# Kernel tuning notes

Measured on AMD Instinct MI355X. Metric: run time of the kernel, lower is better.

## Reference

```python
import jax, jax.numpy as jnp
import numpy as np

# LIFRefracParameters defaults (norse)
TAU_SYN_INV = 200.0   # 1/5e-3
TAU_MEM_INV = 100.0   # 1/1e-2
V_LEAK = 0.0
V_TH = 1.0
V_RESET = 0.0
ALPHA = 100.0
RHO_RESET = 5.0
DT = 0.001


@jax.custom_vjp
def heaviside(x):
    # forward: hard threshold; backward: super-spike surrogate
    return (x > 0).astype(x.dtype)

def _heaviside_fwd(x):
    return heaviside(x), x

def _heaviside_bwd(x, g):
    return (g / (ALPHA * jnp.abs(x) + 1.0) ** 2,)

heaviside.defvjp(_heaviside_fwd, _heaviside_bwd)


def setup_inputs() -> dict:
    key = jax.random.key(0)
    ks = jax.random.split(key, 8)
    B, H, I = 32768, 256, 128
    return {
        "input_tensor": jax.random.normal(ks[0], (B, I), dtype=jnp.float32),
        "z": jax.random.uniform(ks[1], (B, H), dtype=jnp.float32),
        "v": jax.random.normal(ks[2], (B, H), dtype=jnp.float32),
        "i": jax.random.normal(ks[3], (B, H), dtype=jnp.float32),
        "rho": jnp.zeros((B, H), dtype=jnp.float32),
        "input_weights": jax.random.normal(ks[4], (H, I), dtype=jnp.float32) / np.sqrt(I),
        "recurrent_weights": jax.random.normal(ks[5], (H, H), dtype=jnp.float32) / np.sqrt(H),
        "g_coupling": jax.random.normal(ks[6], (H, H), dtype=jnp.float32) / np.sqrt(H),
    }


def reference(input_tensor, z, v, i, rho, input_weights, recurrent_weights, g_coupling):
    # --- lif_mc_step ---
    # membrane decay + multi-compartment coupling
    dv = DT * TAU_MEM_INV * ((V_LEAK - v) + i) + v @ g_coupling.T
    v_decayed = v + dv
    # synaptic current decay
    i_decayed = i + (-DT * TAU_SYN_INV) * i
    # spike
    z_new = heaviside(v_decayed - V_TH)
    v_new = (1.0 - z_new) * v_decayed + z_new * V_RESET
    i_new = i_decayed + input_tensor @ input_weights.T + z @ recurrent_weights.T
    # --- refractory update ---
    refrac_mask = heaviside(rho)
    v_new = (1.0 - refrac_mask) * v_new + refrac_mask * v
    z_new = (1.0 - refrac_mask) * z_new
    rho_new = (1.0 - z_new) * jax.nn.relu(rho - refrac_mask) + z_new * RHO_RESET
    return z_new, v_new, i_new, rho_new
```

## Files before the change

kernel.cpp:

```cpp
#include <hip/hip_runtime.h>

typedef __attribute__((ext_vector_type(8))) _Float16 f16x8;
typedef __attribute__((ext_vector_type(4))) _Float16 f16x4;
typedef __attribute__((ext_vector_type(4))) float    f32x4;

constexpr int Bsz = 32768;
constexpr int Hn  = 256;
constexpr int In  = 128;
constexpr long long BH = (long long)Bsz * Hn;

__global__ __launch_bounds__(256) void k_prep(
    const float* __restrict__ Wi, const float* __restrict__ Wr,
    const float* __restrict__ Gc, _Float16* __restrict__ ws)
{
    const int idx = blockIdx.x * 256 + threadIdx.x;
    {
        const int cg = idx >> 12, rem = idx & 4095;
        const int t = rem >> 9, l = (rem >> 3) & 63, j = idx & 7;
        const int col = cg * 16 + (l & 15);
        const int k   = t * 32 + (l >> 4) * 8 + j;
        float g = Gc[col * Hn + k];
        _Float16 gh = (_Float16)g;
        ws[idx]         = gh;
        ws[65536 + idx] = (_Float16)((g - (float)gh) * 4096.0f);
        ws[131072 + idx] = (_Float16)Wr[col * Hn + k];
    }
    if (idx < 32768) {
        const int cg = idx >> 11, rem = idx & 2047;
        const int t = rem >> 9, l = (rem >> 3) & 63, j = idx & 7;
        const int col = cg * 16 + (l & 15);
        const int k   = t * 32 + (l >> 4) * 8 + j;
        ws[196608 + idx] = (_Float16)Wi[col * In + k];
    }
}

__device__ __forceinline__ int swzH(int row, int colh) {
    return (row * 512 + colh * 2) ^ ((row & 7) << 4);
}
__device__ __forceinline__ int swzX(int row, int colh) {
    return (row * 256 + colh * 2) ^ ((row & 7) << 4);
}
__device__ __forceinline__ int swzO(int row, int col4) {
    return (row * 1024 + col4 * 4) ^ ((row & 7) << 4);
}

__device__ __forceinline__ f16x4 cvt4h(float4 a) {
    f16x4 r;
    r[0] = (_Float16)a.x; r[1] = (_Float16)a.y;
    r[2] = (_Float16)a.z; r[3] = (_Float16)a.w;
    return r;
}
__device__ __forceinline__ f16x4 cvt4m(float4 a) {
    float f[4] = {a.x, a.y, a.z, a.w};
    f16x4 r;
    #pragma unroll
    for (int k = 0; k < 4; ++k) {
        _Float16 h = (_Float16)f[k];
        r[k] = (_Float16)((f[k] - (float)h) * 4096.0f);
    }
    return r;
}

#define MFMA16(A, B, C) __builtin_amdgcn_mfma_f32_16x16x32_f16(A, B, C, 0, 0, 0)

__global__ __launch_bounds__(512, 4) void k_main(
    const float* __restrict__ x, const float* __restrict__ z,
    const float* __restrict__ v, const float* __restrict__ cur,
    const float* __restrict__ rho, const _Float16* __restrict__ ws,
    float* __restrict__ out)
{
    __shared__ char smem[65536];
    char* VH = smem;
    char* VM = smem + 16384;
    char* ZH = smem + 32768;
    char* XH = smem + 49152;
    char* Oc = smem;
    char* Oi = smem + 32768;

    const int tid  = threadIdx.x;
    const int lane = tid & 63;
    const int ln = lane & 15, lg = lane >> 4;
    const int w  = tid >> 6;
    const int rowBase = blockIdx.x * 32;

    {
        const float4* vsrc = (const float4*)(v + (size_t)rowBase * Hn);
        const float4* zsrc = (const float4*)(z + (size_t)rowBase * Hn);
        const float4* xsrc = (const float4*)(x + (size_t)rowBase * In);
        #pragma unroll
        for (int k = 0; k < 4; ++k) {
            const int f = k * 512 + tid;
            const int row = f >> 6, c4 = (f & 63) * 4;
            float4 a = vsrc[f];
            *(f16x4*)(VH + swzH(row, c4)) = cvt4h(a);
            *(f16x4*)(VM + swzH(row, c4)) = cvt4m(a);
        }
        #pragma unroll
        for (int k = 0; k < 4; ++k) {
            const int f = k * 512 + tid;
            const int row = f >> 6, c4 = (f & 63) * 4;
            *(f16x4*)(ZH + swzH(row, c4)) = cvt4h(zsrc[f]);
        }
        #pragma unroll
        for (int k = 0; k < 2; ++k) {
            const int f = k * 512 + tid;
            const int row = f >> 5, c4 = (f & 31) * 4;
            *(f16x4*)(XH + swzX(row, c4)) = cvt4h(xsrc[f]);
        }
    }
    __syncthreads();

    f32x4 acc_c[2][2], acc_cm[2][2], acc_i[2][2];
    #pragma unroll
    for (int m = 0; m < 2; ++m)
        #pragma unroll
        for (int c = 0; c < 2; ++c) {
            acc_c[m][c]  = (f32x4){0.f, 0.f, 0.f, 0.f};
            acc_cm[m][c] = (f32x4){0.f, 0.f, 0.f, 0.f};
            acc_i[m][c]  = (f32x4){0.f, 0.f, 0.f, 0.f};
        }

    const _Float16* Gh  = ws;
    const _Float16* Gm  = ws + 65536;
    const _Float16* Wr  = ws + 131072;
    const _Float16* Wi  = ws + 196608;

    #pragma unroll 2
    for (int t = 0; t < 8; ++t) {
        const int kf = t * 32 + lg * 8;
        f16x8 vh0 = *(const f16x8*)(VH + swzH(ln,      kf));
        f16x8 vh1 = *(const f16x8*)(VH + swzH(ln + 16, kf));
        f16x8 vm0 = *(const f16x8*)(VM + swzH(ln,      kf));
        f16x8 vm1 = *(const f16x8*)(VM + swzH(ln + 16, kf));
        f16x8 zh0 = *(const f16x8*)(ZH + swzH(ln,      kf));
        f16x8 zh1 = *(const f16x8*)(ZH + swzH(ln + 16, kf));
        f16x8 xh0, xh1;
        if (t < 4) {
            xh0 = *(const f16x8*)(XH + swzX(ln,      kf));
            xh1 = *(const f16x8*)(XH + swzX(ln + 16, kf));
        }
        #pragma unroll
        for (int c = 0; c < 2; ++c) {
            const int cg = w * 2 + c;
            f16x8 bgh = *(const f16x8*)(Gh + ((size_t)(cg * 8 + t) * 64 + lane) * 8);
            f16x8 bgm = *(const f16x8*)(Gm + ((size_t)(cg * 8 + t) * 64 + lane) * 8);
            f16x8 bwr = *(const f16x8*)(Wr + ((size_t)(cg * 8 + t) * 64 + lane) * 8);
            acc_c[0][c]  = MFMA16(vh0, bgh, acc_c[0][c]);
            acc_c[1][c]  = MFMA16(vh1, bgh, acc_c[1][c]);
            acc_cm[0][c] = MFMA16(vh0, bgm, acc_cm[0][c]);
            acc_cm[1][c] = MFMA16(vh1, bgm, acc_cm[1][c]);
            acc_cm[0][c] = MFMA16(vm0, bgh, acc_cm[0][c]);
            acc_cm[1][c] = MFMA16(vm1, bgh, acc_cm[1][c]);
            acc_i[0][c]  = MFMA16(zh0, bwr, acc_i[0][c]);
            acc_i[1][c]  = MFMA16(zh1, bwr, acc_i[1][c]);
            if (t < 4) {
                f16x8 bwi = *(const f16x8*)(Wi + ((size_t)(cg * 4 + t) * 64 + lane) * 8);
                acc_i[0][c] = MFMA16(xh0, bwi, acc_i[0][c]);
                acc_i[1][c] = MFMA16(xh1, bwi, acc_i[1][c]);
            }
        }
    }

    #pragma unroll
    for (int m = 0; m < 2; ++m)
        #pragma unroll
        for (int c = 0; c < 2; ++c)
            acc_c[m][c] = acc_c[m][c] + acc_cm[m][c] * 2.44140625e-4f;

    __syncthreads();
    #pragma unroll
    for (int m = 0; m < 2; ++m)
        #pragma unroll
        for (int c = 0; c < 2; ++c) {
            const int col = (w * 2 + c) * 16 + ln;
            #pragma unroll
            for (int r = 0; r < 4; ++r) {
                const int row = m * 16 + lg * 4 + r;
                *(float*)(Oc + swzO(row, col)) = acc_c[m][c][r];
                *(float*)(Oi + swzO(row, col)) = acc_i[m][c][r];
            }
        }

    float4 vv4[4], ii4[4], rh4[4];
    #pragma unroll
    for (int j = 0; j < 4; ++j) {
        const int f = j * 512 + tid;
        const int row = f >> 6, c4 = (f & 63) * 4;
        const size_t gidx = (size_t)(rowBase + row) * Hn + c4;
        vv4[j] = *(const float4*)(v + gidx);
        ii4[j] = *(const float4*)(cur + gidx);
        rh4[j] = *(const float4*)(rho + gidx);
    }
    __syncthreads();

    float* out_z   = out;
    float* out_v   = out + BH;
    float* out_i   = out + 2 * BH;
    float* out_rho = out + 3 * BH;

    #pragma unroll
    for (int j = 0; j < 4; ++j) {
        const int f = j * 512 + tid;
        const int row = f >> 6, c4 = (f & 63) * 4;
        const size_t gidx = (size_t)(rowBase + row) * Hn + c4;
        float4 coup = *(const float4*)(Oc + swzO(row, c4));
        float4 ai   = *(const float4*)(Oi + swzO(row, c4));
        float zn[4], vn[4], rn[4];
        float vvv[4] = {vv4[j].x, vv4[j].y, vv4[j].z, vv4[j].w};
        float iii[4] = {ii4[j].x, ii4[j].y, ii4[j].z, ii4[j].w};
        float rrr[4] = {rh4[j].x, rh4[j].y, rh4[j].z, rh4[j].w};
        float cpp[4] = {coup.x, coup.y, coup.z, coup.w};
        #pragma unroll
        for (int q = 0; q < 4; ++q) {
            float dv   = 0.1f * ((0.0f - vvv[q]) + iii[q]) + cpp[q];
            float vdec = vvv[q] + dv;
            float zf   = (vdec - 1.0f) > 0.0f ? 1.0f : 0.0f;
            float vnew = (1.0f - zf) * vdec;
            float mask = rrr[q] > 0.0f ? 1.0f : 0.0f;
            vnew = (1.0f - mask) * vnew + mask * vvv[q];
            zf   = (1.0f - mask) * zf;
            float rhon = (1.0f - zf) * fmaxf(rrr[q] - mask, 0.0f) + zf * 5.0f;
            zn[q] = zf; vn[q] = vnew; rn[q] = rhon;
        }
        *(float4*)(out_z + gidx)   = make_float4(zn[0], zn[1], zn[2], zn[3]);
        *(float4*)(out_v + gidx)   = make_float4(vn[0], vn[1], vn[2], vn[3]);
        *(float4*)(out_rho + gidx) = make_float4(rn[0], rn[1], rn[2], rn[3]);
        *(float4*)(out_i + gidx)   = make_float4(
            0.8f * iii[0] + ai.x, 0.8f * iii[1] + ai.y,
            0.8f * iii[2] + ai.z, 0.8f * iii[3] + ai.w);
    }
}

extern "C" void kernel_launch(void* const* d_in, const int* in_sizes, int n_in,
                              void* d_out, int out_size, void* d_ws, size_t ws_size,
                              hipStream_t stream) {
    const float* x   = (const float*)d_in[0];
    const float* z   = (const float*)d_in[1];
    const float* v   = (const float*)d_in[2];
    const float* cur = (const float*)d_in[3];
    const float* rho = (const float*)d_in[4];
    const float* Wi  = (const float*)d_in[5];
    const float* Wr  = (const float*)d_in[6];
    const float* Gc  = (const float*)d_in[7];
    float* out = (float*)d_out;
    _Float16* ws = (_Float16*)d_ws;

    hipLaunchKernelGGL(k_prep, dim3(256), dim3(256), 0, stream, Wi, Wr, Gc, ws);
    hipLaunchKernelGGL(k_main, dim3(Bsz / 32), dim3(512), 0, stream,
                       x, z, v, cur, rho, ws, out);
}
```

Measured before the change: 80.78 us.

## Process two row tiles per block with prefetch; write epilogue directly from accumulators

Each block now handles two 32-row tiles. The second tile's v/z/x loads are issued into registers while the first tile's MFMA loop runs, then written to LDS after a barrier. The LDS output staging is removed, so the epilogue reads v/cur/rho and writes results as scalar per-element global accesses from the MFMA accumulator layout. This cuts LDS use and grid size, but loses vectorized, coalesced float4 global stores.

```diff
diff --git a/kernel.cpp b/kernel.cpp
--- a/kernel.cpp
+++ b/kernel.cpp
@@ -40,9 +40,6 @@
 __device__ __forceinline__ int swzX(int row, int colh) {
     return (row * 256 + colh * 2) ^ ((row & 7) << 4);
 }
-__device__ __forceinline__ int swzO(int row, int col4) {
-    return (row * 1024 + col4 * 4) ^ ((row & 7) << 4);
-}
 
 __device__ __forceinline__ f16x4 cvt4h(float4 a) {
     f16x4 r;
@@ -63,172 +60,168 @@
 
 #define MFMA16(A, B, C) __builtin_amdgcn_mfma_f32_16x16x32_f16(A, B, C, 0, 0, 0)
 
+struct SRegs { float4 va[4], za[4], xa[2]; };
+
+__device__ __forceinline__ void ld_regs(
+    int rowBase, int tid,
+    const float* __restrict__ v, const float* __restrict__ z,
+    const float* __restrict__ x, SRegs& R)
+{
+    const float4* vsrc = (const float4*)(v + (size_t)rowBase * Hn);
+    const float4* zsrc = (const float4*)(z + (size_t)rowBase * Hn);
+    const float4* xsrc = (const float4*)(x + (size_t)rowBase * In);
+    #pragma unroll
+    for (int k = 0; k < 4; ++k) R.va[k] = vsrc[k * 512 + tid];
+    #pragma unroll
+    for (int k = 0; k < 4; ++k) R.za[k] = zsrc[k * 512 + tid];
+    #pragma unroll
+    for (int k = 0; k < 2; ++k) R.xa[k] = xsrc[k * 512 + tid];
+}
+
+__device__ __forceinline__ void write_stage(
+    int tid, char* VH, char* VM, char* ZH, char* XH, const SRegs& R)
+{
+    #pragma unroll
+    for (int k = 0; k < 4; ++k) {
+        const int f = k * 512 + tid;
+        const int row = f >> 6, c4 = (f & 63) * 4;
+        *(f16x4*)(VH + swzH(row, c4)) = cvt4h(R.va[k]);
+        *(f16x4*)(VM + swzH(row, c4)) = cvt4m(R.va[k]);
+        *(f16x4*)(ZH + swzH(row, c4)) = cvt4h(R.za[k]);
+    }
+    #pragma unroll
+    for (int k = 0; k < 2; ++k) {
+        const int f = k * 512 + tid;
+        const int row = f >> 5, c4 = (f & 31) * 4;
+        *(f16x4*)(XH + swzX(row, c4)) = cvt4h(R.xa[k]);
+    }
+}
+
 __global__ __launch_bounds__(512, 4) void k_main(
     const float* __restrict__ x, const float* __restrict__ z,
     const float* __restrict__ v, const float* __restrict__ cur,
     const float* __restrict__ rho, const _Float16* __restrict__ ws,
     float* __restrict__ out)
 {
-    __shared__ char smem[65536];
+    __shared__ char smem[57344];
     char* VH = smem;
     char* VM = smem + 16384;
     char* ZH = smem + 32768;
     char* XH = smem + 49152;
-    char* Oc = smem;
-    char* Oi = smem + 32768;
 
     const int tid  = threadIdx.x;
     const int lane = tid & 63;
     const int ln = lane & 15, lg = lane >> 4;
     const int w  = tid >> 6;
-    const int rowBase = blockIdx.x * 32;
-
-    {
-        const float4* vsrc = (const float4*)(v + (size_t)rowBase * Hn);
-        const float4* zsrc = (const float4*)(z + (size_t)rowBase * Hn);
-        const float4* xsrc = (const float4*)(x + (size_t)rowBase * In);
-        #pragma unroll
-        for (int k = 0; k < 4; ++k) {
-            const int f = k * 512 + tid;
-            const int row = f >> 6, c4 = (f & 63) * 4;
-            float4 a = vsrc[f];
-            *(f16x4*)(VH + swzH(row, c4)) = cvt4h(a);
-            *(f16x4*)(VM + swzH(row, c4)) = cvt4m(a);
-        }
-        #pragma unroll
-        for (int k = 0; k < 4; ++k) {
-            const int f = k * 512 + tid;
-            const int row = f >> 6, c4 = (f & 63) * 4;
-            *(f16x4*)(ZH + swzH(row, c4)) = cvt4h(zsrc[f]);
-        }
-        #pragma unroll
-        for (int k = 0; k < 2; ++k) {
-            const int f = k * 512 + tid;
-            const int row = f >> 5, c4 = (f & 31) * 4;
-            *(f16x4*)(XH + swzX(row, c4)) = cvt4h(xsrc[f]);
-        }
-    }
-    __syncthreads();
-
-    f32x4 acc_c[2][2], acc_cm[2][2], acc_i[2][2];
-    #pragma unroll
-    for (int m = 0; m < 2; ++m)
-        #pragma unroll
-        for (int c = 0; c < 2; ++c) {
-            acc_c[m][c]  = (f32x4){0.f, 0.f, 0.f, 0.f};
-            acc_cm[m][c] = (f32x4){0.f, 0.f, 0.f, 0.f};
-            acc_i[m][c]  = (f32x4){0.f, 0.f, 0.f, 0.f};
-        }
+    const int sb0 = blockIdx.x * 64;
+    const int sb1 = sb0 + 32;
 
     const _Float16* Gh  = ws;
     const _Float16* Gm  = ws + 65536;
     const _Float16* Wr  = ws + 131072;
     const _Float16* Wi  = ws + 196608;
 
-    #pragma unroll 2
-    for (int t = 0; t < 8; ++t) {
-        const int kf = t * 32 + lg * 8;
-        f16x8 vh0 = *(const f16x8*)(VH + swzH(ln,      kf));
-        f16x8 vh1 = *(const f16x8*)(VH + swzH(ln + 16, kf));
-        f16x8 vm0 = *(const f16x8*)(VM + swzH(ln,      kf));
-        f16x8 vm1 = *(const f16x8*)(VM + swzH(ln + 16, kf));
-        f16x8 zh0 = *(const f16x8*)(ZH + swzH(ln,      kf));
-        f16x8 zh1 = *(const f16x8*)(ZH + swzH(ln + 16, kf));
-        f16x8 xh0, xh1;
-        if (t < 4) {
-            xh0 = *(const f16x8*)(XH + swzX(ln,      kf));
-            xh1 = *(const f16x8*)(XH + swzX(ln + 16, kf));
-        }
-        #pragma unroll
-        for (int c = 0; c < 2; ++c) {
-            const int cg = w * 2 + c;
-            f16x8 bgh = *(const f16x8*)(Gh + ((size_t)(cg * 8 + t) * 64 + lane) * 8);
-            f16x8 bgm = *(const f16x8*)(Gm + ((size_t)(cg * 8 + t) * 64 + lane) * 8);
-            f16x8 bwr = *(const f16x8*)(Wr + ((size_t)(cg * 8 + t) * 64 + lane) * 8);
-            acc_c[0][c]  = MFMA16(vh0, bgh, acc_c[0][c]);
-            acc_c[1][c]  = MFMA16(vh1, bgh, acc_c[1][c]);
-            acc_cm[0][c] = MFMA16(vh0, bgm, acc_cm[0][c]);
-            acc_cm[1][c] = MFMA16(vh1, bgm, acc_cm[1][c]);
-            acc_cm[0][c] = MFMA16(vm0, bgh, acc_cm[0][c]);
-            acc_cm[1][c] = MFMA16(vm1, bgh, acc_cm[1][c]);
-            acc_i[0][c]  = MFMA16(zh0, bwr, acc_i[0][c]);
-            acc_i[1][c]  = MFMA16(zh1, bwr, acc_i[1][c]);
-            if (t < 4) {
-                f16x8 bwi = *(const f16x8*)(Wi + ((size_t)(cg * 4 + t) * 64 + lane) * 8);
-                acc_i[0][c] = MFMA16(xh0, bwi, acc_i[0][c]);
-                acc_i[1][c] = MFMA16(xh1, bwi, acc_i[1][c]);
-            }
-        }
-    }
-
-    #pragma unroll
-    for (int m = 0; m < 2; ++m)
-        #pragma unroll
-        for (int c = 0; c < 2; ++c)
-            acc_c[m][c] = acc_c[m][c] + acc_cm[m][c] * 2.44140625e-4f;
-
-    __syncthreads();
-    #pragma unroll
-    for (int m = 0; m < 2; ++m)
-        #pragma unroll
-        for (int c = 0; c < 2; ++c) {
-            const int col = (w * 2 + c) * 16 + ln;
-            #pragma unroll
-            for (int r = 0; r < 4; ++r) {
-                const int row = m * 16 + lg * 4 + r;
-                *(float*)(Oc + swzO(row, col)) = acc_c[m][c][r];
-                *(float*)(Oi + swzO(row, col)) = acc_i[m][c][r];
-            }
-        }
-
-    float4 vv4[4], ii4[4], rh4[4];
-    #pragma unroll
-    for (int j = 0; j < 4; ++j) {
-        const int f = j * 512 + tid;
-        const int row = f >> 6, c4 = (f & 63) * 4;
-        const size_t gidx = (size_t)(rowBase + row) * Hn + c4;
-        vv4[j] = *(const float4*)(v + gidx);
-        ii4[j] = *(const float4*)(cur + gidx);
-        rh4[j] = *(const float4*)(rho + gidx);
-    }
-    __syncthreads();
-
     float* out_z   = out;
     float* out_v   = out + BH;
     float* out_i   = out + 2 * BH;
     float* out_rho = out + 3 * BH;
 
-    #pragma unroll
-    for (int j = 0; j < 4; ++j) {
-        const int f = j * 512 + tid;
-        const int row = f >> 6, c4 = (f & 63) * 4;
-        const size_t gidx = (size_t)(rowBase + row) * Hn + c4;
-        float4 coup = *(const float4*)(Oc + swzO(row, c4));
-        float4 ai   = *(const float4*)(Oi + swzO(row, c4));
-        float zn[4], vn[4], rn[4];
-        float vvv[4] = {vv4[j].x, vv4[j].y, vv4[j].z, vv4[j].w};
-        float iii[4] = {ii4[j].x, ii4[j].y, ii4[j].z, ii4[j].w};
-        float rrr[4] = {rh4[j].x, rh4[j].y, rh4[j].z, rh4[j].w};
-        float cpp[4] = {coup.x, coup.y, coup.z, coup.w};
+    auto kloop = [&](f32x4 (&acc_c)[2][2], f32x4 (&acc_cm)[2][2],
+                     f32x4 (&acc_i)[2][2]) {
         #pragma unroll
-        for (int q = 0; q < 4; ++q) {
-            float dv   = 0.1f * ((0.0f - vvv[q]) + iii[q]) + cpp[q];
-            float vdec = vvv[q] + dv;
-            float zf   = (vdec - 1.0f) > 0.0f ? 1.0f : 0.0f;
-            float vnew = (1.0f - zf) * vdec;
-            float mask = rrr[q] > 0.0f ? 1.0f : 0.0f;
-            vnew = (1.0f - mask) * vnew + mask * vvv[q];
-            zf   = (1.0f - mask) * zf;
-            float rhon = (1.0f - zf) * fmaxf(rrr[q] - mask, 0.0f) + zf * 5.0f;
-            zn[q] = zf; vn[q] = vnew; rn[q] = rhon;
+        for (int m = 0; m < 2; ++m)
+            #pragma unroll
+            for (int c = 0; c < 2; ++c) {
+                acc_c[m][c]  = (f32x4){0.f, 0.f, 0.f, 0.f};
+                acc_cm[m][c] = (f32x4){0.f, 0.f, 0.f, 0.f};
+                acc_i[m][c]  = (f32x4){0.f, 0.f, 0.f, 0.f};
+            }
+        #pragma unroll 2
+        for (int t = 0; t < 8; ++t) {
+            const int kf = t * 32 + lg * 8;
+            f16x8 vh0 = *(const f16x8*)(VH + swzH(ln,      kf));
+            f16x8 vh1 = *(const f16x8*)(VH + swzH(ln + 16, kf));
+            f16x8 vm0 = *(const f16x8*)(VM + swzH(ln,      kf));
+            f16x8 vm1 = *(const f16x8*)(VM + swzH(ln + 16, kf));
+            f16x8 zh0 = *(const f16x8*)(ZH + swzH(ln,      kf));
+            f16x8 zh1 = *(const f16x8*)(ZH + swzH(ln + 16, kf));
+            f16x8 xh0, xh1;
+            if (t < 4) {
+                xh0 = *(const f16x8*)(XH + swzX(ln,      kf));
+                xh1 = *(const f16x8*)(XH + swzX(ln + 16, kf));
+            }
+            #pragma unroll
+            for (int c = 0; c < 2; ++c) {
+                const int cg = w * 2 + c;
+                f16x8 bgh = *(const f16x8*)(Gh + ((size_t)(cg * 8 + t) * 64 + lane) * 8);
+                f16x8 bgm = *(const f16x8*)(Gm + ((size_t)(cg * 8 + t) * 64 + lane) * 8);
+                f16x8 bwr = *(const f16x8*)(Wr + ((size_t)(cg * 8 + t) * 64 + lane) * 8);
+                acc_c[0][c]  = MFMA16(vh0, bgh, acc_c[0][c]);
+                acc_c[1][c]  = MFMA16(vh1, bgh, acc_c[1][c]);
+                acc_cm[0][c] = MFMA16(vh0, bgm, acc_cm[0][c]);
+                acc_cm[1][c] = MFMA16(vh1, bgm, acc_cm[1][c]);
+                acc_cm[0][c] = MFMA16(vm0, bgh, acc_cm[0][c]);
+                acc_cm[1][c] = MFMA16(vm1, bgh, acc_cm[1][c]);
+                acc_i[0][c]  = MFMA16(zh0, bwr, acc_i[0][c]);
+                acc_i[1][c]  = MFMA16(zh1, bwr, acc_i[1][c]);
+                if (t < 4) {
+                    f16x8 bwi = *(const f16x8*)(Wi + ((size_t)(cg * 4 + t) * 64 + lane) * 8);
+                    acc_i[0][c] = MFMA16(xh0, bwi, acc_i[0][c]);
+                    acc_i[1][c] = MFMA16(xh1, bwi, acc_i[1][c]);
+                }
+            }
         }
-        *(float4*)(out_z + gidx)   = make_float4(zn[0], zn[1], zn[2], zn[3]);
-        *(float4*)(out_v + gidx)   = make_float4(vn[0], vn[1], vn[2], vn[3]);
-        *(float4*)(out_rho + gidx) = make_float4(rn[0], rn[1], rn[2], rn[3]);
-        *(float4*)(out_i + gidx)   = make_float4(
-            0.8f * iii[0] + ai.x, 0.8f * iii[1] + ai.y,
-            0.8f * iii[2] + ai.z, 0.8f * iii[3] + ai.w);
-    }
+        #pragma unroll
+        for (int m = 0; m < 2; ++m)
+            #pragma unroll
+            for (int c = 0; c < 2; ++c)
+                acc_c[m][c] = acc_c[m][c] + acc_cm[m][c] * 2.44140625e-4f;
+    };
+
+    auto epilogue = [&](int sb, f32x4 (&acc_c)[2][2], f32x4 (&acc_i)[2][2]) {
+        #pragma unroll
+        for (int m = 0; m < 2; ++m)
+            #pragma unroll
+            for (int c = 0; c < 2; ++c) {
+                const int col = (w * 2 + c) * 16 + ln;
+                const int rowb = sb + m * 16 + lg * 4;
+                #pragma unroll
+                for (int r = 0; r < 4; ++r) {
+                    const size_t idx = (size_t)(rowb + r) * Hn + col;
+                    const float vv = v[idx];
+                    const float ii = cur[idx];
+                    const float rh = rho[idx];
+                    float dv   = 0.1f * ((0.0f - vv) + ii) + acc_c[m][c][r];
+                    float vdec = vv + dv;
+                    float zf   = (vdec - 1.0f) > 0.0f ? 1.0f : 0.0f;
+                    float vnew = (1.0f - zf) * vdec;
+                    float mask = rh > 0.0f ? 1.0f : 0.0f;
+                    vnew = (1.0f - mask) * vnew + mask * vv;
+                    zf   = (1.0f - mask) * zf;
+                    float rhon = (1.0f - zf) * fmaxf(rh - mask, 0.0f) + zf * 5.0f;
+                    out_z[idx]   = zf;
+                    out_v[idx]   = vnew;
+                    out_rho[idx] = rhon;
+                    out_i[idx]   = 0.8f * ii + acc_i[m][c][r];
+                }
+            }
+    };
+
+    SRegs R0, R1;
+    ld_regs(sb0, tid, v, z, x, R0);
+    write_stage(tid, VH, VM, ZH, XH, R0);
+    __syncthreads();
+
+    ld_regs(sb1, tid, v, z, x, R1);
+    f32x4 acc_c[2][2], acc_cm[2][2], acc_i[2][2];
+    kloop(acc_c, acc_cm, acc_i);
+    __syncthreads();
+    write_stage(tid, VH, VM, ZH, XH, R1);
+    epilogue(sb0, acc_c, acc_i);
+    __syncthreads();
+
+    kloop(acc_c, acc_cm, acc_i);
+    epilogue(sb1, acc_c, acc_i);
 }
 
 extern "C" void kernel_launch(void* const* d_in, const int* in_sizes, int n_in,
@@ -246,6 +239,6 @@
     _Float16* ws = (_Float16*)d_ws;
 
     hipLaunchKernelGGL(k_prep, dim3(256), dim3(256), 0, stream, Wi, Wr, Gc, ws);
-    hipLaunchKernelGGL(k_main, dim3(Bsz / 32), dim3(512), 0, stream,
+    hipLaunchKernelGGL(k_main, dim3(512), dim3(512), 0, stream,
                        x, z, v, cur, rho, ws, out);
 }
```

New measurement: 115.4 us. 1.43x slower.

## Shrink LDS to 48KB: load x directly from global, stage current output in fp16

Applied to the files above, without the earlier changes.

The x-tile staging buffer in LDS is removed. Each lane now reads its x fragments straight from global memory inside the K loop and converts them to fp16 in registers. The input-current accumulator is written to LDS as fp16 rather than fp32 so it fits in the freed space, and the occupancy hint rises from 4 to 6. The aim is more resident blocks per CU to hide memory latency. The costs are uncoalesced global loads of x in the inner loop and lost precision in the i_new matmul term, which is rounded to fp16 before being added.

```diff
diff --git a/kernel.cpp b/kernel.cpp
--- a/kernel.cpp
+++ b/kernel.cpp
@@ -37,9 +37,6 @@
 __device__ __forceinline__ int swzH(int row, int colh) {
     return (row * 512 + colh * 2) ^ ((row & 7) << 4);
 }
-__device__ __forceinline__ int swzX(int row, int colh) {
-    return (row * 256 + colh * 2) ^ ((row & 7) << 4);
-}
 __device__ __forceinline__ int swzO(int row, int col4) {
     return (row * 1024 + col4 * 4) ^ ((row & 7) << 4);
 }
@@ -60,20 +57,26 @@
     }
     return r;
 }
+__device__ __forceinline__ f16x8 cvt_hi2(float4 a, float4 b) {
+    float f[8] = {a.x, a.y, a.z, a.w, b.x, b.y, b.z, b.w};
+    f16x8 r;
+    #pragma unroll
+    for (int k = 0; k < 8; ++k) r[k] = (_Float16)f[k];
+    return r;
+}
 
 #define MFMA16(A, B, C) __builtin_amdgcn_mfma_f32_16x16x32_f16(A, B, C, 0, 0, 0)
 
-__global__ __launch_bounds__(512, 4) void k_main(
+__global__ __launch_bounds__(512, 6) void k_main(
     const float* __restrict__ x, const float* __restrict__ z,
     const float* __restrict__ v, const float* __restrict__ cur,
     const float* __restrict__ rho, const _Float16* __restrict__ ws,
     float* __restrict__ out)
 {
-    __shared__ char smem[65536];
+    __shared__ char smem[49152];
     char* VH = smem;
     char* VM = smem + 16384;
     char* ZH = smem + 32768;
-    char* XH = smem + 49152;
     char* Oc = smem;
     char* Oi = smem + 32768;
 
@@ -86,7 +89,6 @@
     {
         const float4* vsrc = (const float4*)(v + (size_t)rowBase * Hn);
         const float4* zsrc = (const float4*)(z + (size_t)rowBase * Hn);
-        const float4* xsrc = (const float4*)(x + (size_t)rowBase * In);
         #pragma unroll
         for (int k = 0; k < 4; ++k) {
             const int f = k * 512 + tid;
@@ -101,12 +103,6 @@
             const int row = f >> 6, c4 = (f & 63) * 4;
             *(f16x4*)(ZH + swzH(row, c4)) = cvt4h(zsrc[f]);
         }
-        #pragma unroll
-        for (int k = 0; k < 2; ++k) {
-            const int f = k * 512 + tid;
-            const int row = f >> 5, c4 = (f & 31) * 4;
-            *(f16x4*)(XH + swzX(row, c4)) = cvt4h(xsrc[f]);
-        }
     }
     __syncthreads();
 
@@ -124,6 +120,9 @@
     const _Float16* Gm  = ws + 65536;
     const _Float16* Wr  = ws + 131072;
     const _Float16* Wi  = ws + 196608;
+
+    const float* xr0 = x + (size_t)(rowBase + ln) * In;
+    const float* xr1 = xr0 + 16 * In;
 
     #pragma unroll 2
     for (int t = 0; t < 8; ++t) {
@@ -136,8 +135,12 @@
         f16x8 zh1 = *(const f16x8*)(ZH + swzH(ln + 16, kf));
         f16x8 xh0, xh1;
         if (t < 4) {
-            xh0 = *(const f16x8*)(XH + swzX(ln,      kf));
-            xh1 = *(const f16x8*)(XH + swzX(ln + 16, kf));
+            float4 xa00 = *(const float4*)(xr0 + kf);
+            float4 xa01 = *(const float4*)(xr0 + kf + 4);
+            float4 xa10 = *(const float4*)(xr1 + kf);
+            float4 xa11 = *(const float4*)(xr1 + kf + 4);
+            xh0 = cvt_hi2(xa00, xa01);
+            xh1 = cvt_hi2(xa10, xa11);
         }
         #pragma unroll
         for (int c = 0; c < 2; ++c) {
@@ -177,7 +180,7 @@
             for (int r = 0; r < 4; ++r) {
                 const int row = m * 16 + lg * 4 + r;
                 *(float*)(Oc + swzO(row, col)) = acc_c[m][c][r];
-                *(float*)(Oi + swzO(row, col)) = acc_i[m][c][r];
+                *(_Float16*)(Oi + swzH(row, col)) = (_Float16)acc_i[m][c][r];
             }
         }
 
@@ -204,12 +207,13 @@
         const int row = f >> 6, c4 = (f & 63) * 4;
         const size_t gidx = (size_t)(rowBase + row) * Hn + c4;
         float4 coup = *(const float4*)(Oc + swzO(row, c4));
-        float4 ai   = *(const float4*)(Oi + swzO(row, c4));
+        f16x4 aih   = *(const f16x4*)(Oi + swzH(row, c4));
         float zn[4], vn[4], rn[4];
         float vvv[4] = {vv4[j].x, vv4[j].y, vv4[j].z, vv4[j].w};
         float iii[4] = {ii4[j].x, ii4[j].y, ii4[j].z, ii4[j].w};
         float rrr[4] = {rh4[j].x, rh4[j].y, rh4[j].z, rh4[j].w};
         float cpp[4] = {coup.x, coup.y, coup.z, coup.w};
+        float aif[4] = {(float)aih[0], (float)aih[1], (float)aih[2], (float)aih[3]};
         #pragma unroll
         for (int q = 0; q < 4; ++q) {
             float dv   = 0.1f * ((0.0f - vvv[q]) + iii[q]) + cpp[q];
@@ -226,8 +230,8 @@
         *(float4*)(out_v + gidx)   = make_float4(vn[0], vn[1], vn[2], vn[3]);
         *(float4*)(out_rho + gidx) = make_float4(rn[0], rn[1], rn[2], rn[3]);
         *(float4*)(out_i + gidx)   = make_float4(
-            0.8f * iii[0] + ai.x, 0.8f * iii[1] + ai.y,
-            0.8f * iii[2] + ai.z, 0.8f * iii[3] + ai.w);
+            0.8f * iii[0] + aif[0], 0.8f * iii[1] + aif[1],
+            0.8f * iii[2] + aif[2], 0.8f * iii[3] + aif[3]);
     }
 }
 
```

New measurement: 222.7 us. 2.76x slower.
